# Performance work log

Hardware: AMD Instinct MI355X
Metric: run time of the kernel (lower is better)

## Reference

```python
import jax, jax.numpy as jnp
import numpy as np

K = 9  # ATSS top-k candidates per GT


def cxcywh_to_xyxy(b):
    cx, cy, w, h = b[..., 0], b[..., 1], b[..., 2], b[..., 3]
    return jnp.stack([cx - 0.5 * w, cy - 0.5 * h, cx + 0.5 * w, cy + 0.5 * h], axis=-1)


def elementwise_iou(a, b):
    # a, b: [..., 4] xyxy, broadcastable
    lt = jnp.maximum(a[..., :2], b[..., :2])
    rb = jnp.minimum(a[..., 2:], b[..., 2:])
    wh = jnp.clip(rb - lt, 0.0)
    inter = wh[..., 0] * wh[..., 1]
    area_a = (a[..., 2] - a[..., 0]) * (a[..., 3] - a[..., 1])
    area_b = (b[..., 2] - b[..., 0]) * (b[..., 3] - b[..., 1])
    return inter / (area_a + area_b - inter)


def setup_inputs() -> dict:
    key = jax.random.key(0)
    k1, k2 = jax.random.split(key)
    pred_boxes = jax.random.uniform(k1, (16, 30000, 4), dtype=jnp.float32)
    gt_boxes = jax.random.uniform(k2, (16, 64, 4), dtype=jnp.float32)
    return {"pred_boxes": pred_boxes, "gt_boxes": gt_boxes}


def reference(pred_boxes, gt_boxes):
    # pred_boxes: [B, N, 4] cxcywh; gt_boxes: [B, G, 4] cxcywh
    G = gt_boxes.shape[1]

    def per_image(pred, gt):
        # center-distance matrix [G, N] (the cdist in the original)
        diff = gt[:, None, :2] - pred[None, :, :2]
        dist = jnp.sqrt(jnp.sum(diff * diff, axis=-1))
        # k smallest distances per GT
        _, k_idx = jax.lax.top_k(-dist, K)          # [G, K]
        k_boxes = pred[k_idx]                        # [G, K, 4]
        gt_xyxy = cxcywh_to_xyxy(gt)                 # [G, 4]
        kb_xyxy = cxcywh_to_xyxy(k_boxes)            # [G, K, 4]
        ious = elementwise_iou(gt_xyxy[:, None, :], kb_xyxy)  # [G, K]
        # adaptive threshold: mean + std (torch.std is unbiased -> ddof=1)
        thr = jnp.mean(ious, axis=1, keepdims=True) + jnp.std(ious, axis=1, ddof=1, keepdims=True)
        cx, cy = k_boxes[..., 0], k_boxes[..., 1]
        inside = ((gt_xyxy[:, None, 0] <= cx) & (cx <= gt_xyxy[:, None, 2]) &
                  (gt_xyxy[:, None, 1] <= cy) & (cy <= gt_xyxy[:, None, 3]))
        mask = (ious >= thr) & inside                # [G, K]
        # padded index representation (original returns ragged lists):
        pred_idx = jnp.where(mask, k_idx, -1)
        gt_idx = jnp.where(mask, jnp.arange(G, dtype=jnp.int64)[:, None], -1)
        return pred_idx, gt_idx, mask, ious

    return jax.vmap(per_image)(pred_boxes, gt_boxes)
```

## Files before the change

### kernel.cpp

```cpp
#include <hip/hip_runtime.h>
#include <stdint.h>

typedef unsigned long long u64;

#define KCAND 9
#define BATCH 16
#define NPRED 30000
#define NGT   64
#define TPB   512
#define GTA   4
#define UNRF  4
#define PPT   (TPB * UNRF * 2)
#define NT    8
#define PSTR  32768
#define NF4   (PSTR / 2)
#define CAP   128
#define INITKEY 0x7F800000FFFFFFFFULL
#define FINF  __uint_as_float(0x7F800000u)
#define SENT  (~0ULL)

__device__ __forceinline__ float wave_min_f(float v) {
#pragma unroll
    for (int s = 1; s < 64; s <<= 1) v = fminf(v, __shfl_xor(v, s, 64));
    return v;
}
__device__ __forceinline__ u64 wave_min_u64(u64 v) {
#pragma unroll
    for (int s = 1; s < 64; s <<= 1) {
        u64 o = __shfl_xor(v, s, 64);
        v = o < v ? o : v;
    }
    return v;
}

__global__ __launch_bounds__(256) void compact_xy(
    const float* __restrict__ pred, float2* __restrict__ xy)
{
    int e = blockIdx.x * 256 + threadIdx.x;
    int b = e >> 15;
    int i = e & (PSTR - 1);
    float2 v;
    if (i < NPRED) {
        float4 p = ((const float4*)pred)[(size_t)b * NPRED + i];
        v = make_float2(p.x, p.y);
    } else {
        v = make_float2(FINF, FINF);
    }
    xy[e] = v;
}

#define DIST(GX, GY, PX, PY, D)                                              \
    { float _dx = __fsub_rn(GX, PX), _dy = __fsub_rn(GY, PY);                \
      D = __fadd_rn(__fmul_rn(_dx, _dx), __fmul_rn(_dy, _dy)); }

template <bool PADDED>
__global__ __launch_bounds__(TPB, 2) void atss4(
    const float2* __restrict__ xy,
    const float*  __restrict__ pred,
    const float*  __restrict__ gt,
    float* __restrict__ out)
{
#pragma clang fp contract(off)
    const int tid  = threadIdx.x;
    const int lane = tid & 63;
    const int wv   = tid >> 6;

    const int bi = blockIdx.x;
    const int b  = (bi & 7) + 8 * (bi >> 7);
    const int g0 = ((bi >> 3) & 15) * GTA;

    const float4* gt4 = (const float4*)gt;
    const int w0 = b * NGT + g0;
    const float4 gq0 = gt4[w0],     gq1 = gt4[w0 + 1];
    const float4 gq2 = gt4[w0 + 2], gq3 = gt4[w0 + 3];
    const float aX = gq0.x, aY = gq0.y;
    const float bX = gq1.x, bY = gq1.y;
    const float cX = gq2.x, cY = gq2.y;
    const float dX = gq3.x, dY = gq3.y;

    const float4* p4 = (const float4*)pred + (size_t)b * NPRED;
    const float2* x2 = PADDED ? (xy + (size_t)b * PSTR) : (const float2*)0;
    const float4* x4 = (const float4*)x2;

    __shared__ float tmins[GTA][TPB];
    __shared__ float tg[GTA];
    __shared__ int   cnt[GTA];
    __shared__ u64   cand[GTA][CAP];

    if (tid < GTA) cnt[tid] = 0;

    float lm0 = FINF, lm1 = FINF, lm2 = FINF, lm3 = FINF;
#define P1(PX, PY)                                                           \
    { float d;                                                               \
      DIST(aX, aY, PX, PY, d); lm0 = fminf(lm0, d);                          \
      DIST(bX, bY, PX, PY, d); lm1 = fminf(lm1, d);                          \
      DIST(cX, cY, PX, PY, d); lm2 = fminf(lm2, d);                          \
      DIST(dX, dY, PX, PY, d); lm3 = fminf(lm3, d); }

    if (PADDED) {
        for (int t = 0; t < NT; ++t) {
            const int f0 = t * (PPT / 2) + tid;
#pragma unroll
            for (int k = 0; k < UNRF; ++k) {
                float4 q = x4[f0 + k * TPB];
                P1(q.x, q.y) P1(q.z, q.w)
            }
        }
    } else {
        for (int t = 0; t < NT; ++t) {
#pragma unroll
            for (int j = 0; j < 2 * UNRF; ++j) {
                const int i = t * PPT + j * TPB + tid;
                const bool vv = i < NPRED;
                float4 q = p4[vv ? i : 0];
                float px = vv ? q.x : FINF, py = vv ? q.y : FINF;
                P1(px, py)
            }
        }
    }
#undef P1

    tmins[0][tid] = lm0; tmins[1][tid] = lm1;
    tmins[2][tid] = lm2; tmins[3][tid] = lm3;
    __syncthreads();

    if (wv < GTA) {
        float a[TPB / 64];
#pragma unroll
        for (int j = 0; j < TPB / 64; ++j) a[j] = tmins[wv][j * 64 + lane];
        float T = FINF;
#pragma unroll
        for (int r = 0; r < KCAND; ++r) {
            float ml = a[0];
#pragma unroll
            for (int j = 1; j < TPB / 64; ++j) ml = fminf(ml, a[j]);
            float m = wave_min_f(ml);
#pragma unroll
            for (int j = 0; j < TPB / 64; ++j) a[j] = (a[j] == m) ? FINF : a[j];
            T = m;
        }
        if (lane == 0) tg[wv] = T;
    }
    __syncthreads();
    const float T0 = tg[0], T1 = tg[1], T2 = tg[2], T3 = tg[3];

#define COLLECT(H, D, C, IDXE)                                               \
    { u64 bm = __ballot(H);                                                  \
      if (bm) {                                                              \
          int ldr = __ffsll(bm) - 1;                                         \
          int base = 0;                                                      \
          if (lane == ldr) base = atomicAdd(&cnt[C], (int)__popcll(bm));     \
          base = __shfl(base, ldr, 64);                                      \
          if (H) {                                                           \
              int src = lane;                                                \
              int slot = base + (int)__popcll(bm & ((1ULL << lane) - 1ULL)); \
              if (slot < CAP)                                                \
                  cand[C][slot] =                                            \
                      ((u64)__float_as_uint(D) << 32) | (unsigned)(IDXE);    \
          } } }
#define P2(PX, PY, IDXE)                                                     \
    { float e0, e1, e2, e3;                                                  \
      DIST(aX, aY, PX, PY, e0); DIST(bX, bY, PX, PY, e1);                    \
      DIST(cX, cY, PX, PY, e2); DIST(dX, dY, PX, PY, e3);                    \
      bool h0 = e0 <= T0, h1 = e1 <= T1, h2 = e2 <= T2, h3 = e3 <= T3;       \
      if (__ballot(h0 | h1 | h2 | h3)) {                                     \
          COLLECT(h0, e0, 0, IDXE) COLLECT(h1, e1, 1, IDXE)                  \
          COLLECT(h2, e2, 2, IDXE) COLLECT(h3, e3, 3, IDXE)                  \
      } }

    if (PADDED) {
        for (int t = 0; t < NT; ++t) {
            const int f0 = t * (PPT / 2) + tid;
            const int fw = t * (PPT / 2) + (tid - lane);
#pragma unroll
            for (int k = 0; k < UNRF; ++k) {
                float4 q = x4[f0 + k * TPB];
                P2(q.x, q.y, 2 * (fw + k * TPB + src))
                P2(q.z, q.w, 2 * (fw + k * TPB + src) + 1)
            }
        }
    } else {
        for (int t = 0; t < NT; ++t) {
#pragma unroll
            for (int j = 0; j < 2 * UNRF; ++j) {
                const int i = t * PPT + j * TPB + tid;
                const int iw = t * PPT + j * TPB + (tid - lane);
                const bool vv = i < NPRED;
                float4 q = p4[vv ? i : 0];
                float px = vv ? q.x : FINF, py = vv ? q.y : FINF;
                P2(px, py, iw + src)
            }
        }
    }
#undef P2
#undef COLLECT
    __syncthreads();

    if (wv >= GTA) return;
    const int c = wv;
    const float gX = (c == 0) ? aX : (c == 1) ? bX : (c == 2) ? cX : dX;
    const float gY = (c == 0) ? aY : (c == 1) ? bY : (c == 2) ? cY : dY;
    const int n = cnt[c];

    u64 fin = SENT;
    if (n <= CAP) {
        u64 k0 = (lane < n)      ? cand[c][lane]      : SENT;
        u64 k1 = (lane + 64 < n) ? cand[c][lane + 64] : SENT;
#pragma unroll
        for (int r = 0; r < KCAND; ++r) {
            u64 ml = k0 < k1 ? k0 : k1;
            u64 m = wave_min_u64(ml);
            if (lane == r) fin = m;
            if (k0 == m) k0 = SENT;
            if (k1 == m) k1 = SENT;
        }
    } else {
        u64 val = INITKEY;
        float Tf = tg[c];
        for (int i0 = 0; i0 < PSTR; i0 += 64) {
            const int i = i0 + lane;
            float px, py;
            if (PADDED) {
                float2 p = x2[i];  px = p.x;  py = p.y;
            } else {
                const bool vv = i < NPRED;
                float4 q = p4[vv ? i : 0];
                px = vv ? q.x : FINF;  py = vv ? q.y : FINF;
            }
            float d;  DIST(gX, gY, px, py, d);
            u64 pend = __ballot(d <= Tf);
            while (pend) {
                const int src = __ffsll(pend) - 1;
                pend &= pend - 1;
                const unsigned kd = __shfl(__float_as_uint(d), src, 64);
                const unsigned ki = (unsigned)(i0 + src);
                const u64 key = ((u64)kd << 32) | ki;
                u64 Tkey = __shfl(val, 8, 64);
                if (key < Tkey) {
                    const u64 ltm = __ballot(val < key) & 0x1FFULL;
                    const int pos = __popcll(ltm);
                    const u64 sh = __shfl_up(val, 1, 64);
                    if (lane < KCAND) {
                        if (lane == pos)      val = key;
                        else if (lane > pos)  val = sh;
                    }
                    Tkey = __shfl(val, 8, 64);
                    Tf = fminf(tg[c], __uint_as_float((unsigned)(Tkey >> 32)));
                    pend &= __ballot(d <= Tf);
                }
            }
        }
        fin = val;
    }

    const int g = g0 + c;
    const int w = b * NGT + g;
    const float4 gq = gt4[w];
    const float gcx = gq.x, gcy = gq.y;

    const bool active = (lane < KCAND);
    const unsigned idx = active ? (unsigned)(fin & 0xffffffffu) : 0u;

    float4 pbx = p4[idx];

    float gx1 = gcx - 0.5f * gq.z, gy1 = gcy - 0.5f * gq.w;
    float gx2 = gcx + 0.5f * gq.z, gy2 = gcy + 0.5f * gq.w;
    float kx1 = pbx.x - 0.5f * pbx.z, ky1 = pbx.y - 0.5f * pbx.w;
    float kx2 = pbx.x + 0.5f * pbx.z, ky2 = pbx.y + 0.5f * pbx.w;

    float ltx = fmaxf(gx1, kx1), lty = fmaxf(gy1, ky1);
    float rbx = fminf(gx2, kx2), rby = fminf(gy2, ky2);
    float wvd = fmaxf(rbx - ltx, 0.0f);
    float hvd = fmaxf(rby - lty, 0.0f);
    float inter  = wvd * hvd;
    float area_a = (gx2 - gx1) * (gy2 - gy1);
    float area_b = (kx2 - kx1) * (ky2 - ky1);
    float iou = inter / ((area_a + area_b) - inter);

    float v = active ? iou : 0.0f;
    float s = v;
#pragma unroll
    for (int m = 1; m < 64; m <<= 1) s += __shfl_xor(s, m, 64);
    float mean = s / 9.0f;

    float dev = active ? (iou - mean) : 0.0f;
    float ss = dev * dev;
#pragma unroll
    for (int m = 1; m < 64; m <<= 1) ss += __shfl_xor(ss, m, 64);
    float stdv = sqrtf(ss / 8.0f);
    float thr = mean + stdv;

    bool inside = (gx1 <= pbx.x) && (pbx.x <= gx2) &&
                  (gy1 <= pbx.y) && (pbx.y <= gy2);
    bool maskk = (iou >= thr) && inside;

    if (active) {
        const size_t chunk = (size_t)BATCH * NGT * KCAND;
        const size_t o = (size_t)w * KCAND + lane;
        out[0 * chunk + o] = maskk ? (float)idx : -1.0f;
        out[1 * chunk + o] = maskk ? (float)g   : -1.0f;
        out[2 * chunk + o] = maskk ? 1.0f : 0.0f;
        out[3 * chunk + o] = iou;
    }
}

extern "C" void kernel_launch(void* const* d_in, const int* in_sizes, int n_in,
                              void* d_out, int out_size, void* d_ws, size_t ws_size,
                              hipStream_t stream) {
    const float* pred = (const float*)d_in[0];
    const float* gtb  = (const float*)d_in[1];
    float* out = (float*)d_out;

    const size_t need = (size_t)BATCH * PSTR * sizeof(float2);
    if (ws_size >= need) {
        float2* xy = (float2*)d_ws;
        compact_xy<<<BATCH * PSTR / 256, 256, 0, stream>>>(pred, xy);
        atss4<true><<<BATCH * (NGT / GTA), TPB, 0, stream>>>(xy, pred, gtb, out);
    } else {
        atss4<false><<<BATCH * (NGT / GTA), TPB, 0, stream>>>(
            nullptr, pred, gtb, out);
    }
}
```

Before: 83.62 us.

## Rank predictions by expanded squared-distance surrogate using precomputed half-norms

Replaces the per-GT squared distance in both scan passes with the surrogate 0.5|p|^2 - g·p. That costs two FMAs per GT instead of sub/mul/add chains, and the per-prediction half-norm is precomputed in the compaction kernel. Exact distances are recomputed only for the candidates being collected, and thresholds gain a small margin so rounding in the surrogate does not drop true neighbours. This adds an extra per-prediction float stream to read and a mismatch between the surrogate threshold and the fallback-path threshold, which is rescaled and could admit more candidates or risk inexact ranking.

New measurement: 83.75 us. About the same (+0.1%).

```diff
diff --git a/kernel.cpp b/kernel.cpp
--- a/kernel.cpp
+++ b/kernel.cpp
@@ -13,10 +13,11 @@
 #define PPT   (TPB * UNRF * 2)
 #define NT    8
 #define PSTR  32768
-#define NF4   (PSTR / 2)
 #define CAP   128
+#define SMARG 1e-5f
 #define INITKEY 0x7F800000FFFFFFFFULL
 #define FINF  __uint_as_float(0x7F800000u)
+#define FNAN  __uint_as_float(0x7FC00000u)
 #define SENT  (~0ULL)
 
 __device__ __forceinline__ float wave_min_f(float v) {
@@ -33,20 +34,24 @@
     return v;
 }
 
-__global__ __launch_bounds__(256) void compact_xy(
-    const float* __restrict__ pred, float2* __restrict__ xy)
+__global__ __launch_bounds__(256) void compact_xyr(
+    const float* __restrict__ pred, float2* __restrict__ xy,
+    float* __restrict__ rr)
 {
     int e = blockIdx.x * 256 + threadIdx.x;
     int b = e >> 15;
     int i = e & (PSTR - 1);
-    float2 v;
+    float2 v; float r;
     if (i < NPRED) {
         float4 p = ((const float4*)pred)[(size_t)b * NPRED + i];
         v = make_float2(p.x, p.y);
+        r = __fadd_rn(__fmul_rn(0.5f * p.x, p.x), __fmul_rn(0.5f * p.y, p.y));
     } else {
         v = make_float2(FINF, FINF);
+        r = FNAN;
     }
     xy[e] = v;
+    rr[e] = r;
 }
 
 #define DIST(GX, GY, PX, PY, D)                                              \
@@ -56,6 +61,7 @@
 template <bool PADDED>
 __global__ __launch_bounds__(TPB, 2) void atss4(
     const float2* __restrict__ xy,
+    const float*  __restrict__ rr,
     const float*  __restrict__ pred,
     const float*  __restrict__ gt,
     float* __restrict__ out)
@@ -77,10 +83,14 @@
     const float bX = gq1.x, bY = gq1.y;
     const float cX = gq2.x, cY = gq2.y;
     const float dX = gq3.x, dY = gq3.y;
+    const float nAx = -aX, nAy = -aY, nBx = -bX, nBy = -bY;
+    const float nCx = -cX, nCy = -cY, nDx = -dX, nDy = -dY;
 
     const float4* p4 = (const float4*)pred + (size_t)b * NPRED;
     const float2* x2 = PADDED ? (xy + (size_t)b * PSTR) : (const float2*)0;
     const float4* x4 = (const float4*)x2;
+    const float2* r2 = PADDED ? (const float2*)(rr + (size_t)b * PSTR)
+                              : (const float2*)0;
 
     __shared__ float tmins[GTA][TPB];
     __shared__ float tg[GTA];
@@ -90,20 +100,20 @@
     if (tid < GTA) cnt[tid] = 0;
 
     float lm0 = FINF, lm1 = FINF, lm2 = FINF, lm3 = FINF;
-#define P1(PX, PY)                                                           \
-    { float d;                                                               \
-      DIST(aX, aY, PX, PY, d); lm0 = fminf(lm0, d);                          \
-      DIST(bX, bY, PX, PY, d); lm1 = fminf(lm1, d);                          \
-      DIST(cX, cY, PX, PY, d); lm2 = fminf(lm2, d);                          \
-      DIST(dX, dY, PX, PY, d); lm3 = fminf(lm3, d); }
+#define S1(PX, PY, R)                                                        \
+    { lm0 = fminf(lm0, fmaf(nAx, PX, fmaf(nAy, PY, R)));                     \
+      lm1 = fminf(lm1, fmaf(nBx, PX, fmaf(nBy, PY, R)));                     \
+      lm2 = fminf(lm2, fmaf(nCx, PX, fmaf(nCy, PY, R)));                     \
+      lm3 = fminf(lm3, fmaf(nDx, PX, fmaf(nDy, PY, R))); }
 
     if (PADDED) {
         for (int t = 0; t < NT; ++t) {
             const int f0 = t * (PPT / 2) + tid;
 #pragma unroll
             for (int k = 0; k < UNRF; ++k) {
-                float4 q = x4[f0 + k * TPB];
-                P1(q.x, q.y) P1(q.z, q.w)
+                float4 q  = x4[f0 + k * TPB];
+                float2 rv = r2[f0 + k * TPB];
+                S1(q.x, q.y, rv.x) S1(q.z, q.w, rv.y)
             }
         }
     } else {
@@ -113,12 +123,14 @@
                 const int i = t * PPT + j * TPB + tid;
                 const bool vv = i < NPRED;
                 float4 q = p4[vv ? i : 0];
-                float px = vv ? q.x : FINF, py = vv ? q.y : FINF;
-                P1(px, py)
-            }
-        }
-    }
-#undef P1
+                float px = q.x, py = q.y;
+                float r = vv ? __fadd_rn(__fmul_rn(0.5f * px, px),
+                                         __fmul_rn(0.5f * py, py)) : FNAN;
+                S1(px, py, r)
+            }
+        }
+    }
+#undef S1
 
     tmins[0][tid] = lm0; tmins[1][tid] = lm1;
     tmins[2][tid] = lm2; tmins[3][tid] = lm3;
@@ -139,12 +151,12 @@
             for (int j = 0; j < TPB / 64; ++j) a[j] = (a[j] == m) ? FINF : a[j];
             T = m;
         }
-        if (lane == 0) tg[wv] = T;
+        if (lane == 0) tg[wv] = T + SMARG;
     }
     __syncthreads();
     const float T0 = tg[0], T1 = tg[1], T2 = tg[2], T3 = tg[3];
 
-#define COLLECT(H, D, C, IDXE)                                               \
+#define COLLECT(H, GX, GY, C, PX, PY, IDXE)                                  \
     { u64 bm = __ballot(H);                                                  \
       if (bm) {                                                              \
           int ldr = __ffsll(bm) - 1;                                         \
@@ -152,31 +164,34 @@
           if (lane == ldr) base = atomicAdd(&cnt[C], (int)__popcll(bm));     \
           base = __shfl(base, ldr, 64);                                      \
           if (H) {                                                           \
-              int src = lane;                                                \
+              float dd; DIST(GX, GY, PX, PY, dd);                            \
               int slot = base + (int)__popcll(bm & ((1ULL << lane) - 1ULL)); \
               if (slot < CAP)                                                \
                   cand[C][slot] =                                            \
-                      ((u64)__float_as_uint(D) << 32) | (unsigned)(IDXE);    \
+                      ((u64)__float_as_uint(dd) << 32) | (unsigned)(IDXE);   \
           } } }
-#define P2(PX, PY, IDXE)                                                     \
-    { float e0, e1, e2, e3;                                                  \
-      DIST(aX, aY, PX, PY, e0); DIST(bX, bY, PX, PY, e1);                    \
-      DIST(cX, cY, PX, PY, e2); DIST(dX, dY, PX, PY, e3);                    \
-      bool h0 = e0 <= T0, h1 = e1 <= T1, h2 = e2 <= T2, h3 = e3 <= T3;       \
+#define S2(PX, PY, R, IDXE)                                                  \
+    { float s0 = fmaf(nAx, PX, fmaf(nAy, PY, R));                            \
+      float s1 = fmaf(nBx, PX, fmaf(nBy, PY, R));                            \
+      float s2 = fmaf(nCx, PX, fmaf(nCy, PY, R));                            \
+      float s3 = fmaf(nDx, PX, fmaf(nDy, PY, R));                            \
+      bool h0 = s0 <= T0, h1 = s1 <= T1, h2 = s2 <= T2, h3 = s3 <= T3;       \
       if (__ballot(h0 | h1 | h2 | h3)) {                                     \
-          COLLECT(h0, e0, 0, IDXE) COLLECT(h1, e1, 1, IDXE)                  \
-          COLLECT(h2, e2, 2, IDXE) COLLECT(h3, e3, 3, IDXE)                  \
+          COLLECT(h0, aX, aY, 0, PX, PY, IDXE)                               \
+          COLLECT(h1, bX, bY, 1, PX, PY, IDXE)                               \
+          COLLECT(h2, cX, cY, 2, PX, PY, IDXE)                               \
+          COLLECT(h3, dX, dY, 3, PX, PY, IDXE)                               \
       } }
 
     if (PADDED) {
         for (int t = 0; t < NT; ++t) {
             const int f0 = t * (PPT / 2) + tid;
-            const int fw = t * (PPT / 2) + (tid - lane);
 #pragma unroll
             for (int k = 0; k < UNRF; ++k) {
-                float4 q = x4[f0 + k * TPB];
-                P2(q.x, q.y, 2 * (fw + k * TPB + src))
-                P2(q.z, q.w, 2 * (fw + k * TPB + src) + 1)
+                float4 q  = x4[f0 + k * TPB];
+                float2 rv = r2[f0 + k * TPB];
+                S2(q.x, q.y, rv.x, 2 * (f0 + k * TPB))
+                S2(q.z, q.w, rv.y, 2 * (f0 + k * TPB) + 1)
             }
         }
     } else {
@@ -184,15 +199,16 @@
 #pragma unroll
             for (int j = 0; j < 2 * UNRF; ++j) {
                 const int i = t * PPT + j * TPB + tid;
-                const int iw = t * PPT + j * TPB + (tid - lane);
                 const bool vv = i < NPRED;
                 float4 q = p4[vv ? i : 0];
-                float px = vv ? q.x : FINF, py = vv ? q.y : FINF;
-                P2(px, py, iw + src)
-            }
-        }
-    }
-#undef P2
+                float px = q.x, py = q.y;
+                float r = vv ? __fadd_rn(__fmul_rn(0.5f * px, px),
+                                         __fmul_rn(0.5f * py, py)) : FNAN;
+                S2(px, py, r, i)
+            }
+        }
+    }
+#undef S2
 #undef COLLECT
     __syncthreads();
 
@@ -215,8 +231,11 @@
             if (k1 == m) k1 = SENT;
         }
     } else {
+        const float Chat = __fadd_rn(__fmul_rn(0.5f * gX, gX),
+                                     __fmul_rn(0.5f * gY, gY));
+        const float Tcap = 2.0f * (tg[c] + Chat) + 1e-4f;
         u64 val = INITKEY;
-        float Tf = tg[c];
+        float Tf = Tcap;
         for (int i0 = 0; i0 < PSTR; i0 += 64) {
             const int i = i0 + lane;
             float px, py;
@@ -245,7 +264,7 @@
                         else if (lane > pos)  val = sh;
                     }
                     Tkey = __shfl(val, 8, 64);
-                    Tf = fminf(tg[c], __uint_as_float((unsigned)(Tkey >> 32)));
+                    Tf = fminf(Tcap, __uint_as_float((unsigned)(Tkey >> 32)));
                     pend &= __ballot(d <= Tf);
                 }
             }
@@ -311,13 +330,16 @@
     const float* gtb  = (const float*)d_in[1];
     float* out = (float*)d_out;
 
-    const size_t need = (size_t)BATCH * PSTR * sizeof(float2);
+    const size_t nxy  = (size_t)BATCH * PSTR * sizeof(float2);
+    const size_t need = nxy + (size_t)BATCH * PSTR * sizeof(float);
     if (ws_size >= need) {
         float2* xy = (float2*)d_ws;
-        compact_xy<<<BATCH * PSTR / 256, 256, 0, stream>>>(pred, xy);
-        atss4<true><<<BATCH * (NGT / GTA), TPB, 0, stream>>>(xy, pred, gtb, out);
+        float*  rr = (float*)((char*)d_ws + nxy);
+        compact_xyr<<<BATCH * PSTR / 256, 256, 0, stream>>>(pred, xy, rr);
+        atss4<true><<<BATCH * (NGT / GTA), TPB, 0, stream>>>(
+            xy, rr, pred, gtb, out);
     } else {
         atss4<false><<<BATCH * (NGT / GTA), TPB, 0, stream>>>(
-            nullptr, pred, gtb, out);
-    }
-}
+            nullptr, nullptr, pred, gtb, out);
+    }
+}
```

## Drop compaction pre-pass; use 2 GTs per 256-thread block reading float4 preds

Applied to the files above, without the earlier changes.

Removes the separate compact_xy kernel that wrote padded xy pairs to the workspace, so the main kernel reads the original float4 prediction boxes directly. Each block now handles 2 ground-truth boxes with 256 threads instead of 4 with 512, doubling the block count to 512. The loops are simplified to two strided loads per iteration with bounds masking. This saves a launch and a workspace write/read, but each prediction is re-read by twice as many blocks and the float4 loads fetch unused w/h data.

New measurement: 94.65 us. +13.2%, slower.

```diff
diff --git a/kernel.cpp b/kernel.cpp
--- a/kernel.cpp
+++ b/kernel.cpp
@@ -2,18 +2,14 @@
 #include <stdint.h>
 
 typedef unsigned long long u64;
+typedef unsigned int u32;
 
 #define KCAND 9
 #define BATCH 16
 #define NPRED 30000
 #define NGT   64
-#define TPB   512
-#define GTA   4
-#define UNRF  4
-#define PPT   (TPB * UNRF * 2)
-#define NT    8
-#define PSTR  32768
-#define NF4   (PSTR / 2)
+#define TPB   256
+#define GTA   2
 #define CAP   128
 #define INITKEY 0x7F800000FFFFFFFFULL
 #define FINF  __uint_as_float(0x7F800000u)
@@ -33,31 +29,13 @@
     return v;
 }
 
-__global__ __launch_bounds__(256) void compact_xy(
-    const float* __restrict__ pred, float2* __restrict__ xy)
-{
-    int e = blockIdx.x * 256 + threadIdx.x;
-    int b = e >> 15;
-    int i = e & (PSTR - 1);
-    float2 v;
-    if (i < NPRED) {
-        float4 p = ((const float4*)pred)[(size_t)b * NPRED + i];
-        v = make_float2(p.x, p.y);
-    } else {
-        v = make_float2(FINF, FINF);
-    }
-    xy[e] = v;
-}
-
 #define DIST(GX, GY, PX, PY, D)                                              \
     { float _dx = __fsub_rn(GX, PX), _dy = __fsub_rn(GY, PY);                \
       D = __fadd_rn(__fmul_rn(_dx, _dx), __fmul_rn(_dy, _dy)); }
 
-template <bool PADDED>
-__global__ __launch_bounds__(TPB, 2) void atss4(
-    const float2* __restrict__ xy,
-    const float*  __restrict__ pred,
-    const float*  __restrict__ gt,
+__global__ __launch_bounds__(TPB, 2) void atss2(
+    const float* __restrict__ pred,
+    const float* __restrict__ gt,
     float* __restrict__ out)
 {
 #pragma clang fp contract(off)
@@ -66,21 +44,16 @@
     const int wv   = tid >> 6;
 
     const int bi = blockIdx.x;
-    const int b  = (bi & 7) + 8 * (bi >> 7);
-    const int g0 = ((bi >> 3) & 15) * GTA;
+    const int b  = (bi & 7) + 8 * (bi >> 8);
+    const int g0 = ((bi >> 3) & 31) * GTA;
 
     const float4* gt4 = (const float4*)gt;
-    const int w0 = b * NGT + g0;
-    const float4 gq0 = gt4[w0],     gq1 = gt4[w0 + 1];
-    const float4 gq2 = gt4[w0 + 2], gq3 = gt4[w0 + 3];
-    const float aX = gq0.x, aY = gq0.y;
-    const float bX = gq1.x, bY = gq1.y;
-    const float cX = gq2.x, cY = gq2.y;
-    const float dX = gq3.x, dY = gq3.y;
+    const float4 gA = gt4[b * NGT + g0];
+    const float4 gB = gt4[b * NGT + g0 + 1];
+    const float aX = gA.x, aY = gA.y;
+    const float bX = gB.x, bY = gB.y;
 
     const float4* p4 = (const float4*)pred + (size_t)b * NPRED;
-    const float2* x2 = PADDED ? (xy + (size_t)b * PSTR) : (const float2*)0;
-    const float4* x4 = (const float4*)x2;
 
     __shared__ float tmins[GTA][TPB];
     __shared__ float tg[GTA];
@@ -89,39 +62,22 @@
 
     if (tid < GTA) cnt[tid] = 0;
 
-    float lm0 = FINF, lm1 = FINF, lm2 = FINF, lm3 = FINF;
-#define P1(PX, PY)                                                           \
-    { float d;                                                               \
-      DIST(aX, aY, PX, PY, d); lm0 = fminf(lm0, d);                          \
-      DIST(bX, bY, PX, PY, d); lm1 = fminf(lm1, d);                          \
-      DIST(cX, cY, PX, PY, d); lm2 = fminf(lm2, d);                          \
-      DIST(dX, dY, PX, PY, d); lm3 = fminf(lm3, d); }
-
-    if (PADDED) {
-        for (int t = 0; t < NT; ++t) {
-            const int f0 = t * (PPT / 2) + tid;
-#pragma unroll
-            for (int k = 0; k < UNRF; ++k) {
-                float4 q = x4[f0 + k * TPB];
-                P1(q.x, q.y) P1(q.z, q.w)
-            }
-        }
-    } else {
-        for (int t = 0; t < NT; ++t) {
-#pragma unroll
-            for (int j = 0; j < 2 * UNRF; ++j) {
-                const int i = t * PPT + j * TPB + tid;
-                const bool vv = i < NPRED;
-                float4 q = p4[vv ? i : 0];
-                float px = vv ? q.x : FINF, py = vv ? q.y : FINF;
-                P1(px, py)
-            }
-        }
-    }
-#undef P1
-
-    tmins[0][tid] = lm0; tmins[1][tid] = lm1;
-    tmins[2][tid] = lm2; tmins[3][tid] = lm3;
+    float lmA = FINF, lmB = FINF;
+    for (int i0 = 0; i0 < NPRED; i0 += 2 * TPB) {
+        const int i = i0 + tid;
+        float4 q0 = p4[i];
+        float d;
+        DIST(aX, aY, q0.x, q0.y, d); lmA = fminf(lmA, d);
+        DIST(bX, bY, q0.x, q0.y, d); lmB = fminf(lmB, d);
+        const int i2 = i + TPB;
+        const bool vv = i2 < NPRED;
+        float4 q1 = p4[vv ? i2 : 0];
+        DIST(aX, aY, q1.x, q1.y, d); lmA = fminf(lmA, vv ? d : FINF);
+        DIST(bX, bY, q1.x, q1.y, d); lmB = fminf(lmB, vv ? d : FINF);
+    }
+
+    tmins[0][tid] = lmA;
+    tmins[1][tid] = lmB;
     __syncthreads();
 
     if (wv < GTA) {
@@ -142,9 +98,9 @@
         if (lane == 0) tg[wv] = T;
     }
     __syncthreads();
-    const float T0 = tg[0], T1 = tg[1], T2 = tg[2], T3 = tg[3];
-
-#define COLLECT(H, D, C, IDXE)                                               \
+    const float T0 = tg[0], T1 = tg[1];
+
+#define COLLECT(H, D, C, IDX)                                                \
     { u64 bm = __ballot(H);                                                  \
       if (bm) {                                                              \
           int ldr = __ffsll(bm) - 1;                                         \
@@ -152,54 +108,42 @@
           if (lane == ldr) base = atomicAdd(&cnt[C], (int)__popcll(bm));     \
           base = __shfl(base, ldr, 64);                                      \
           if (H) {                                                           \
-              int src = lane;                                                \
               int slot = base + (int)__popcll(bm & ((1ULL << lane) - 1ULL)); \
               if (slot < CAP)                                                \
                   cand[C][slot] =                                            \
-                      ((u64)__float_as_uint(D) << 32) | (unsigned)(IDXE);    \
+                      ((u64)__float_as_uint(D) << 32) | (unsigned)(IDX);     \
           } } }
-#define P2(PX, PY, IDXE)                                                     \
-    { float e0, e1, e2, e3;                                                  \
-      DIST(aX, aY, PX, PY, e0); DIST(bX, bY, PX, PY, e1);                    \
-      DIST(cX, cY, PX, PY, e2); DIST(dX, dY, PX, PY, e3);                    \
-      bool h0 = e0 <= T0, h1 = e1 <= T1, h2 = e2 <= T2, h3 = e3 <= T3;       \
-      if (__ballot(h0 | h1 | h2 | h3)) {                                     \
-          COLLECT(h0, e0, 0, IDXE) COLLECT(h1, e1, 1, IDXE)                  \
-          COLLECT(h2, e2, 2, IDXE) COLLECT(h3, e3, 3, IDXE)                  \
-      } }
-
-    if (PADDED) {
-        for (int t = 0; t < NT; ++t) {
-            const int f0 = t * (PPT / 2) + tid;
-            const int fw = t * (PPT / 2) + (tid - lane);
-#pragma unroll
-            for (int k = 0; k < UNRF; ++k) {
-                float4 q = x4[f0 + k * TPB];
-                P2(q.x, q.y, 2 * (fw + k * TPB + src))
-                P2(q.z, q.w, 2 * (fw + k * TPB + src) + 1)
-            }
-        }
-    } else {
-        for (int t = 0; t < NT; ++t) {
-#pragma unroll
-            for (int j = 0; j < 2 * UNRF; ++j) {
-                const int i = t * PPT + j * TPB + tid;
-                const int iw = t * PPT + j * TPB + (tid - lane);
-                const bool vv = i < NPRED;
-                float4 q = p4[vv ? i : 0];
-                float px = vv ? q.x : FINF, py = vv ? q.y : FINF;
-                P2(px, py, iw + src)
-            }
-        }
-    }
-#undef P2
+
+    for (int i0 = 0; i0 < NPRED; i0 += 2 * TPB) {
+        const int i = i0 + tid;
+        float4 q0 = p4[i];
+        float e0, e1;
+        DIST(aX, aY, q0.x, q0.y, e0);
+        DIST(bX, bY, q0.x, q0.y, e1);
+        bool h0 = e0 <= T0, h1 = e1 <= T1;
+        if (__ballot(h0 | h1)) {
+            COLLECT(h0, e0, 0, i)
+            COLLECT(h1, e1, 1, i)
+        }
+        const int i2 = i + TPB;
+        const bool vv = i2 < NPRED;
+        float4 q1 = p4[vv ? i2 : 0];
+        DIST(aX, aY, q1.x, q1.y, e0);
+        DIST(bX, bY, q1.x, q1.y, e1);
+        h0 = vv && (e0 <= T0);
+        h1 = vv && (e1 <= T1);
+        if (__ballot(h0 | h1)) {
+            COLLECT(h0, e0, 0, i2)
+            COLLECT(h1, e1, 1, i2)
+        }
+    }
 #undef COLLECT
     __syncthreads();
 
     if (wv >= GTA) return;
     const int c = wv;
-    const float gX = (c == 0) ? aX : (c == 1) ? bX : (c == 2) ? cX : dX;
-    const float gY = (c == 0) ? aY : (c == 1) ? bY : (c == 2) ? cY : dY;
+    const float gX = c ? bX : aX;
+    const float gY = c ? bY : aY;
     const int n = cnt[c];
 
     u64 fin = SENT;
@@ -217,17 +161,13 @@
     } else {
         u64 val = INITKEY;
         float Tf = tg[c];
-        for (int i0 = 0; i0 < PSTR; i0 += 64) {
+        for (int i0 = 0; i0 < NPRED; i0 += 64) {
             const int i = i0 + lane;
-            float px, py;
-            if (PADDED) {
-                float2 p = x2[i];  px = p.x;  py = p.y;
-            } else {
-                const bool vv = i < NPRED;
-                float4 q = p4[vv ? i : 0];
-                px = vv ? q.x : FINF;  py = vv ? q.y : FINF;
-            }
-            float d;  DIST(gX, gY, px, py, d);
+            const bool vv = i < NPRED;
+            float4 q = p4[vv ? i : 0];
+            float d;
+            DIST(gX, gY, q.x, q.y, d);
+            if (!vv) d = FINF;
             u64 pend = __ballot(d <= Tf);
             while (pend) {
                 const int src = __ffsll(pend) - 1;
@@ -255,7 +195,7 @@
 
     const int g = g0 + c;
     const int w = b * NGT + g;
-    const float4 gq = gt4[w];
+    const float4 gq = c ? gB : gA;
     const float gcx = gq.x, gcy = gq.y;
 
     const bool active = (lane < KCAND);
@@ -310,14 +250,7 @@
     const float* pred = (const float*)d_in[0];
     const float* gtb  = (const float*)d_in[1];
     float* out = (float*)d_out;
-
-    const size_t need = (size_t)BATCH * PSTR * sizeof(float2);
-    if (ws_size >= need) {
-        float2* xy = (float2*)d_ws;
-        compact_xy<<<BATCH * PSTR / 256, 256, 0, stream>>>(pred, xy);
-        atss4<true><<<BATCH * (NGT / GTA), TPB, 0, stream>>>(xy, pred, gtb, out);
-    } else {
-        atss4<false><<<BATCH * (NGT / GTA), TPB, 0, stream>>>(
-            nullptr, pred, gtb, out);
-    }
-}
+    (void)d_ws; (void)ws_size;
+
+    atss2<<<BATCH * (NGT / GTA), TPB, 0, stream>>>(pred, gtb, out);
+}
```
